# Optimization experiments

Measured on AMD Instinct MI355X. Metric: run time of the kernel, lower is better.

Reference implementation:

```python
import jax, jax.numpy as jnp
import numpy as np

B, A, H, E = 64, 512, 128, 16384  # batch, nodes(amino acids), hidden, edges


def setup_inputs() -> dict:
    key = jax.random.key(0)
    ks = jax.random.split(key, 8)
    s = 1.0 / np.sqrt(H)
    return {
        "x": jax.random.normal(ks[0], (B, A, H), dtype=jnp.float32),
        "pos": jax.random.normal(ks[1], (B, A, 3), dtype=jnp.float32),
        "edge_index": jax.random.randint(ks[2], (2, E), 0, A, dtype=jnp.int64),
        "w1": jax.random.normal(ks[3], (H, H), dtype=jnp.float32) * s,
        "b1": jnp.zeros((H,), dtype=jnp.float32),
        "w2": jax.random.normal(ks[4], (H, H), dtype=jnp.float32) * s,
        "b2": jnp.zeros((H,), dtype=jnp.float32),
        "wfc": jax.random.normal(ks[5], (A * H, 1), dtype=jnp.float32) / np.sqrt(A * H),
        "bfc": jnp.zeros((1,), dtype=jnp.float32),
    }


def reference(x, pos, edge_index, w1, b1, w2, b2, wfc, bfc):
    # pos / edge_attr: the original computes a cdist edge_attr but message() ignores it.
    src = edge_index[0]
    dst = edge_index[1]
    # gather neighbor features along node dim: [B, E, H]
    xj = x[:, src, :]
    # per-edge MLP: Linear-ReLU-Linear
    msg = jnp.maximum(jnp.einsum('beh,hk->bek', xj, w1) + b1, 0.0)
    msg = jnp.einsum('bek,kh->beh', msg, w2) + b2
    # scatter-mean back to target nodes
    agg = jnp.zeros_like(x).at[:, dst, :].add(msg)  # [B, A, H]
    cnt = jnp.zeros((x.shape[1],), x.dtype).at[dst].add(1.0)
    agg = agg / jnp.maximum(cnt, 1.0)[None, :, None]
    # flatten + final linear -> [B, 1]
    flat = agg.reshape(agg.shape[0], -1)
    return flat @ wfc + bfc
```

## Files before the change

kernel.cpp:

```cpp
#include <hip/hip_runtime.h>

#define Hdim   128
#define Anodes 512
#define Bbatch 64
#define Eedges 16384
#define AMASK  (Anodes - 1)

#define WS_W1T  0
#define WS_U    8192
#define WS_CARR 73728

typedef __attribute__((ext_vector_type(8))) short short8;
typedef __attribute__((ext_vector_type(4))) float f32x4;

__device__ __forceinline__ short f2bf(float f) {
    union { float f; unsigned u; } v; v.f = f;
    unsigned r = v.u + 0x7FFFu + ((v.u >> 16) & 1u);
    return (short)(r >> 16);
}

__global__ __launch_bounds__(512)
void k_G(const int* __restrict__ ei, const float* __restrict__ w1,
         const float* __restrict__ w2, const float* __restrict__ wfc,
         const float* __restrict__ b2, const float* __restrict__ bfc,
         float* __restrict__ ws, float* __restrict__ out) {
    __shared__ float w2L[Hdim][Hdim + 1];
    __shared__ unsigned short dl[1024];
    __shared__ unsigned cntL[Anodes];
    __shared__ float plist[1024];
    __shared__ float Gr[Hdim];
    __shared__ float qred[4][Hdim];
    __shared__ int nz;
    __shared__ int sawS;

    const int tid = threadIdx.x;
    const int s = blockIdx.x;

    if (s >= Anodes) {
        if (s < Anodes + 4) {
            const int k0 = (s - Anodes) * 32;
            for (int i = tid; i < 32 * 128; i += 512) {
                int r = i >> 7, c = i & 127;
                w2L[r][c] = w1[(k0 + r) * Hdim + c];
            }
            __syncthreads();
            if (tid < 256) {
                short* o = (short*)(ws + WS_W1T);
                const int n = tid >> 1, j0 = (tid & 1) * 16;
                short tmp[16];
                #pragma unroll
                for (int j = 0; j < 16; ++j) tmp[j] = f2bf(w2L[j0 + j][n]);
                short8* dst = (short8*)(o + n * Hdim + k0 + j0);
                dst[0] = *(short8*)(tmp);
                dst[1] = *(short8*)(tmp + 8);
            }
        } else {
            if (tid < Bbatch) out[tid] = bfc[0];
        }
        return;
    }

    for (int i = tid; i < Anodes; i += 512) cntL[i] = 0u;
    if (tid == 0) { nz = 0; sawS = 0; }
    __syncthreads();

    {
        const float4* w2v = (const float4*)w2;
        for (int i = tid; i < (Hdim * Hdim) / 4; i += 512) {
            float4 v = w2v[i];
            float* dst = &w2L[i >> 5][(i & 31) * 4];
            dst[0] = v.x; dst[1] = v.y; dst[2] = v.z; dst[3] = v.w;
        }
    }

    const int4* s4 = (const int4*)ei;
    const int4* d4 = (const int4*)(ei + Eedges);
    for (int i = tid; i < Eedges / 4; i += 512) {
        int4 sv = s4[i];
        int4 dv = d4[i];
        int d;
        d = dv.x & AMASK; atomicAdd(&cntL[d], 1u); if (d == s) sawS = 1;
        if ((sv.x & AMASK) == s) dl[atomicAdd(&nz, 1)] = (unsigned short)d;
        d = dv.y & AMASK; atomicAdd(&cntL[d], 1u); if (d == s) sawS = 1;
        if ((sv.y & AMASK) == s) dl[atomicAdd(&nz, 1)] = (unsigned short)d;
        d = dv.z & AMASK; atomicAdd(&cntL[d], 1u); if (d == s) sawS = 1;
        if ((sv.z & AMASK) == s) dl[atomicAdd(&nz, 1)] = (unsigned short)d;
        d = dv.w & AMASK; atomicAdd(&cntL[d], 1u); if (d == s) sawS = 1;
        if ((sv.w & AMASK) == s) dl[atomicAdd(&nz, 1)] = (unsigned short)d;
    }
    __syncthreads();
    const int n = nz;
    for (int i = tid; i < n; i += 512)
        plist[i] = 1.0f / fmaxf((float)cntL[dl[i]], 1.0f);
    __syncthreads();

    const int k = tid & 127, q = tid >> 7;
    float g = 0.f;
    for (int i = q; i < n; i += 4)
        g += plist[i] * wfc[(size_t)dl[i] * Hdim + k];
    qred[q][k] = g;
    __syncthreads();
    if (q == 0) Gr[k] = qred[0][k] + qred[1][k] + qred[2][k] + qred[3][k];
    __syncthreads();

    float u = 0.f;
    const int h0 = q * 32;
    #pragma unroll 8
    for (int hh = h0; hh < h0 + 32; ++hh) u += w2L[k][hh] * Gr[hh];
    qred[q][k] = u;
    __syncthreads();
    if (q == 0) ws[WS_U + (size_t)s * Hdim + k] = qred[0][k] + qred[1][k] + qred[2][k] + qred[3][k];

    float cv = 0.f;
    if (tid < 128) cv = b2[tid] * wfc[(size_t)s * Hdim + tid];
    #pragma unroll
    for (int off = 32; off; off >>= 1) cv += __shfl_down(cv, off, 64);
    __syncthreads();
    if (tid == 0)  qred[0][0] = cv;
    if (tid == 64) qred[0][1] = cv;
    __syncthreads();
    if (tid == 0) ws[WS_CARR + s] = sawS ? (qred[0][0] + qred[0][1]) : 0.f;
}

__global__ __launch_bounds__(256)
void k_main(const float* __restrict__ x, const float* __restrict__ b1,
            const float* __restrict__ ws, float* __restrict__ out) {
    __shared__ short w1s[Hdim * Hdim];
    __shared__ float red[4];

    const int tid  = threadIdx.x;
    const int row0 = blockIdx.x * 64;
    const int b    = blockIdx.x >> 3;
    const int a0   = (blockIdx.x & 7) * 64;

    {
        const short8* gsrc = (const short8*)(ws + WS_W1T);
        for (int i = tid; i < 2048; i += 256) {
            short8 v = gsrc[i];
            int n = i >> 4;
            int byte = (i * 16) ^ ((n & 7) << 4);
            *(short8*)((char*)w1s + byte) = v;
        }
    }
    __syncthreads();

    const int w = tid >> 6;
    const int l = tid & 63;
    const int c = l & 15;
    const int g = l >> 4;

    const float* xrow = x + (size_t)(row0 + w * 16 + c) * Hdim;

    f32x4 acc[8];
    #pragma unroll
    for (int n = 0; n < 8; ++n) acc[n] = (f32x4){0.f, 0.f, 0.f, 0.f};

    #pragma unroll
    for (int ks = 0; ks < 4; ++ks) {
        const int k0 = ks * 32;
        float4 a_lo = *(const float4*)(xrow + k0 + 8 * g);
        float4 a_hi = *(const float4*)(xrow + k0 + 8 * g + 4);
        short8 a;
        a[0] = f2bf(a_lo.x); a[1] = f2bf(a_lo.y); a[2] = f2bf(a_lo.z); a[3] = f2bf(a_lo.w);
        a[4] = f2bf(a_hi.x); a[5] = f2bf(a_hi.y); a[6] = f2bf(a_hi.z); a[7] = f2bf(a_hi.w);
        #pragma unroll
        for (int n = 0; n < 8; ++n) {
            int byte = (((n * 16 + c) << 8) + ((k0 + 8 * g) << 1)) ^ ((c & 7) << 4);
            short8 bf = *(short8*)((char*)w1s + byte);
            acc[n] = __builtin_amdgcn_mfma_f32_16x16x32_bf16(a, bf, acc[n], 0, 0, 0);
        }
    }

    float part = 0.f;
    const float* U = ws + WS_U;
    #pragma unroll
    for (int n = 0; n < 8; ++n) {
        const int colg = n * 16 + c;
        const float bv = b1[colg];
        #pragma unroll
        for (int r = 0; r < 4; ++r) {
            const int arow = a0 + w * 16 + g * 4 + r;
            float z = acc[n][r] + bv;
            part += fmaxf(z, 0.f) * U[arow * Hdim + colg];
        }
    }
    #pragma unroll
    for (int off = 32; off; off >>= 1) part += __shfl_down(part, off, 64);
    if (l == 0) red[w] = part;
    __syncthreads();

    float cw = 0.f;
    if (tid < 64) cw = ws[WS_CARR + a0 + tid];
    #pragma unroll
    for (int off = 32; off; off >>= 1) cw += __shfl_down(cw, off, 64);
    if (tid == 0)
        atomicAdd(out + b, red[0] + red[1] + red[2] + red[3] + cw);
}

extern "C" void kernel_launch(void* const* d_in, const int* in_sizes, int n_in,
                              void* d_out, int out_size, void* d_ws, size_t ws_size,
                              hipStream_t stream) {
    const float* x   = (const float*)d_in[0];
    const int*   ei  = (const int*)d_in[2];
    const float* w1  = (const float*)d_in[3];
    const float* b1  = (const float*)d_in[4];
    const float* w2  = (const float*)d_in[5];
    const float* b2  = (const float*)d_in[6];
    const float* wfc = (const float*)d_in[7];
    const float* bfc = (const float*)d_in[8];
    float* out = (float*)d_out;
    float* ws  = (float*)d_ws;

    hipLaunchKernelGGL(k_G,    dim3(517), dim3(512), 0, stream,
                       ei, w1, w2, wfc, b2, bfc, ws, out);
    hipLaunchKernelGGL(k_main, dim3(512), dim3(256), 0, stream, x, b1, ws, out);
}
```

Baseline: 24.24 us.

## Process two source nodes per k_G block to halve redundant edge scans

Each k_G block now handles two source nodes with 1024 threads, so the full edge-index scan, the per-node in-degree counting and the w2 load into shared memory happen once per pair instead of once per node. The grid shrinks from 517 to 261 blocks. This cuts redundant global reads and LDS atomics on cntL, at the cost of larger blocks, more LDS per block and extra branching in the scan loop.

```diff
diff --git a/kernel.cpp b/kernel.cpp
--- a/kernel.cpp
+++ b/kernel.cpp
@@ -19,27 +19,27 @@
     return (short)(r >> 16);
 }
 
-__global__ __launch_bounds__(512)
+__global__ __launch_bounds__(1024)
 void k_G(const int* __restrict__ ei, const float* __restrict__ w1,
          const float* __restrict__ w2, const float* __restrict__ wfc,
          const float* __restrict__ b2, const float* __restrict__ bfc,
          float* __restrict__ ws, float* __restrict__ out) {
     __shared__ float w2L[Hdim][Hdim + 1];
-    __shared__ unsigned short dl[1024];
+    __shared__ unsigned short dl[2][1024];
     __shared__ unsigned cntL[Anodes];
-    __shared__ float plist[1024];
-    __shared__ float Gr[Hdim];
-    __shared__ float qred[4][Hdim];
-    __shared__ int nz;
-    __shared__ int sawS;
+    __shared__ float plist[2][1024];
+    __shared__ float Gr[2][Hdim];
+    __shared__ float qred[2][4][Hdim];
+    __shared__ int nz[2];
+    __shared__ int saw[2];
 
     const int tid = threadIdx.x;
-    const int s = blockIdx.x;
-
-    if (s >= Anodes) {
-        if (s < Anodes + 4) {
-            const int k0 = (s - Anodes) * 32;
-            for (int i = tid; i < 32 * 128; i += 512) {
+    const int blk = blockIdx.x;
+
+    if (blk >= 256) {
+        if (blk < 260) {
+            const int k0 = (blk - 256) * 32;
+            for (int i = tid; i < 32 * 128; i += 1024) {
                 int r = i >> 7, c = i & 127;
                 w2L[r][c] = w1[(k0 + r) * Hdim + c];
             }
@@ -60,13 +60,15 @@
         return;
     }
 
-    for (int i = tid; i < Anodes; i += 512) cntL[i] = 0u;
-    if (tid == 0) { nz = 0; sawS = 0; }
+    const int s0 = blk * 2;
+
+    for (int i = tid; i < Anodes; i += 1024) cntL[i] = 0u;
+    if (tid < 2) { nz[tid] = 0; saw[tid] = 0; }
     __syncthreads();
 
     {
         const float4* w2v = (const float4*)w2;
-        for (int i = tid; i < (Hdim * Hdim) / 4; i += 512) {
+        for (int i = tid; i < (Hdim * Hdim) / 4; i += 1024) {
             float4 v = w2v[i];
             float* dst = &w2L[i >> 5][(i & 31) * 4];
             dst[0] = v.x; dst[1] = v.y; dst[2] = v.z; dst[3] = v.w;
@@ -75,51 +77,68 @@
 
     const int4* s4 = (const int4*)ei;
     const int4* d4 = (const int4*)(ei + Eedges);
-    for (int i = tid; i < Eedges / 4; i += 512) {
+    for (int i = tid; i < Eedges / 4; i += 1024) {
         int4 sv = s4[i];
         int4 dv = d4[i];
-        int d;
-        d = dv.x & AMASK; atomicAdd(&cntL[d], 1u); if (d == s) sawS = 1;
-        if ((sv.x & AMASK) == s) dl[atomicAdd(&nz, 1)] = (unsigned short)d;
-        d = dv.y & AMASK; atomicAdd(&cntL[d], 1u); if (d == s) sawS = 1;
-        if ((sv.y & AMASK) == s) dl[atomicAdd(&nz, 1)] = (unsigned short)d;
-        d = dv.z & AMASK; atomicAdd(&cntL[d], 1u); if (d == s) sawS = 1;
-        if ((sv.z & AMASK) == s) dl[atomicAdd(&nz, 1)] = (unsigned short)d;
-        d = dv.w & AMASK; atomicAdd(&cntL[d], 1u); if (d == s) sawS = 1;
-        if ((sv.w & AMASK) == s) dl[atomicAdd(&nz, 1)] = (unsigned short)d;
-    }
-    __syncthreads();
-    const int n = nz;
-    for (int i = tid; i < n; i += 512)
-        plist[i] = 1.0f / fmaxf((float)cntL[dl[i]], 1.0f);
-    __syncthreads();
-
-    const int k = tid & 127, q = tid >> 7;
+        int d, ss;
+        d = dv.x & AMASK; atomicAdd(&cntL[d], 1u);
+        if (d == s0) saw[0] = 1; else if (d == s0 + 1) saw[1] = 1;
+        ss = sv.x & AMASK;
+        if (ss == s0) dl[0][atomicAdd(&nz[0], 1)] = (unsigned short)d;
+        else if (ss == s0 + 1) dl[1][atomicAdd(&nz[1], 1)] = (unsigned short)d;
+        d = dv.y & AMASK; atomicAdd(&cntL[d], 1u);
+        if (d == s0) saw[0] = 1; else if (d == s0 + 1) saw[1] = 1;
+        ss = sv.y & AMASK;
+        if (ss == s0) dl[0][atomicAdd(&nz[0], 1)] = (unsigned short)d;
+        else if (ss == s0 + 1) dl[1][atomicAdd(&nz[1], 1)] = (unsigned short)d;
+        d = dv.z & AMASK; atomicAdd(&cntL[d], 1u);
+        if (d == s0) saw[0] = 1; else if (d == s0 + 1) saw[1] = 1;
+        ss = sv.z & AMASK;
+        if (ss == s0) dl[0][atomicAdd(&nz[0], 1)] = (unsigned short)d;
+        else if (ss == s0 + 1) dl[1][atomicAdd(&nz[1], 1)] = (unsigned short)d;
+        d = dv.w & AMASK; atomicAdd(&cntL[d], 1u);
+        if (d == s0) saw[0] = 1; else if (d == s0 + 1) saw[1] = 1;
+        ss = sv.w & AMASK;
+        if (ss == s0) dl[0][atomicAdd(&nz[0], 1)] = (unsigned short)d;
+        else if (ss == s0 + 1) dl[1][atomicAdd(&nz[1], 1)] = (unsigned short)d;
+    }
+    __syncthreads();
+
+    const int h  = tid >> 9;
+    const int t5 = tid & 511;
+    const int n  = nz[h];
+    for (int i = t5; i < n; i += 512)
+        plist[h][i] = 1.0f / fmaxf((float)cntL[dl[h][i]], 1.0f);
+    __syncthreads();
+
+    const int k = tid & 127, q = (tid >> 7) & 3;
     float g = 0.f;
     for (int i = q; i < n; i += 4)
-        g += plist[i] * wfc[(size_t)dl[i] * Hdim + k];
-    qred[q][k] = g;
-    __syncthreads();
-    if (q == 0) Gr[k] = qred[0][k] + qred[1][k] + qred[2][k] + qred[3][k];
+        g += plist[h][i] * wfc[(size_t)dl[h][i] * Hdim + k];
+    qred[h][q][k] = g;
+    __syncthreads();
+    if (q == 0) Gr[h][k] = qred[h][0][k] + qred[h][1][k] + qred[h][2][k] + qred[h][3][k];
     __syncthreads();
 
     float u = 0.f;
     const int h0 = q * 32;
     #pragma unroll 8
-    for (int hh = h0; hh < h0 + 32; ++hh) u += w2L[k][hh] * Gr[hh];
-    qred[q][k] = u;
-    __syncthreads();
-    if (q == 0) ws[WS_U + (size_t)s * Hdim + k] = qred[0][k] + qred[1][k] + qred[2][k] + qred[3][k];
+    for (int hh = h0; hh < h0 + 32; ++hh) u += w2L[k][hh] * Gr[h][hh];
+    qred[h][q][k] = u;
+    __syncthreads();
+    if (q == 0)
+        ws[WS_U + (size_t)(s0 + h) * Hdim + k] =
+            qred[h][0][k] + qred[h][1][k] + qred[h][2][k] + qred[h][3][k];
 
     float cv = 0.f;
-    if (tid < 128) cv = b2[tid] * wfc[(size_t)s * Hdim + tid];
+    if (t5 < 128) cv = b2[t5] * wfc[(size_t)(s0 + h) * Hdim + t5];
     #pragma unroll
     for (int off = 32; off; off >>= 1) cv += __shfl_down(cv, off, 64);
     __syncthreads();
-    if (tid == 0)  qred[0][0] = cv;
-    if (tid == 64) qred[0][1] = cv;
-    __syncthreads();
-    if (tid == 0) ws[WS_CARR + s] = sawS ? (qred[0][0] + qred[0][1]) : 0.f;
+    if (t5 == 0)  qred[h][0][0] = cv;
+    if (t5 == 64) qred[h][0][1] = cv;
+    __syncthreads();
+    if (t5 == 0) ws[WS_CARR + s0 + h] = saw[h] ? (qred[h][0][0] + qred[h][0][1]) : 0.f;
 }
 
 __global__ __launch_bounds__(256)
@@ -211,7 +230,7 @@
     float* out = (float*)d_out;
     float* ws  = (float*)d_ws;
 
-    hipLaunchKernelGGL(k_G,    dim3(517), dim3(512), 0, stream,
+    hipLaunchKernelGGL(k_G,    dim3(261), dim3(1024), 0, stream,
                        ei, w1, w2, wfc, b2, bfc, ws, out);
     hipLaunchKernelGGL(k_main, dim3(512), dim3(256), 0, stream, x, b1, ws, out);
 }
```

Result: faster. 23.20 us, median of 2 (-4.3%).
